# Kernel tuning notes

Measured on AMD Instinct MI355X. Metric: run time of the kernel, lower is better.

## Reference

```python
import jax, jax.numpy as jnp
import numpy as np

N = 100000      # number of entities
E = 400000      # number of edges (before self-loops)
D = 200         # feature_dim
D0 = 100        # init_fea_dim
NREL = 475      # 2*num_rels + 1 (self-loop relation = NREL-1)
NBR = 100       # num_base_r
B = 1024        # query batch
L = 2           # number of cells / layers
EPS = 1e-5


def _bn(x, g, b):
    # BatchNorm1d, training-mode batch statistics (biased var), per-feature affine
    m = jnp.mean(x, axis=0)
    v = jnp.var(x, axis=0)
    return (x - m) * jax.lax.rsqrt(v + EPS) * g + b


def setup_inputs() -> dict:
    key = jax.random.key(0)
    ks = jax.random.split(key, 12)
    return {
        # graph (edge list form of the DGL graph g)
        "src_id": jax.random.randint(ks[0], (E,), 0, N),
        "dst_id": jax.random.randint(ks[1], (E,), 0, N),
        "e_type": jax.random.randint(ks[2], (E,), 0, NREL - 1),  # NREL-1 reserved for self-loop
        # link-prediction queries
        "subj": jax.random.randint(ks[3], (B,), 0, N),
        "rel": jax.random.randint(ks[4], (B,), 0, NREL),
        # learned parameters
        "emb_h": jax.random.normal(ks[5], (N, D0), dtype=jnp.float32) * 0.02,
        "emb_e": jax.random.normal(ks[6], (NBR, D), dtype=jnp.float32) * 0.1,
        "lin_w": jax.random.normal(ks[7], (D0, D), dtype=jnp.float32) * (1.0 / np.sqrt(D0)),
        "lin_b": jnp.zeros((D,), dtype=jnp.float32),
        "rel_wt": jax.random.normal(ks[8], (NREL, NBR), dtype=jnp.float32) * 0.1,
        "w_rel": jax.random.normal(ks[9], (D, D), dtype=jnp.float32) * (1.0 / np.sqrt(D)),
        # per-cell params, stacked over L layers
        "agg_bn_g": jnp.ones((L, D), dtype=jnp.float32),
        "agg_bn_b": jnp.zeros((L, D), dtype=jnp.float32),
        "cell_bn_g": jnp.ones((L, D), dtype=jnp.float32),
        "cell_bn_b": jnp.zeros((L, D), dtype=jnp.float32),
        "concat_w": jax.random.normal(ks[10], (L, D, D), dtype=jnp.float32) * (1.0 / np.sqrt(D)),
        "concat_b": jnp.zeros((L, D), dtype=jnp.float32),
    }


def reference(src_id, dst_id, e_type, subj, rel,
              emb_h, emb_e, lin_w, lin_b, rel_wt, w_rel,
              agg_bn_g, agg_bn_b, cell_bn_g, cell_bn_b, concat_w, concat_b):
    nodes = jnp.arange(N, dtype=src_id.dtype)
    # append self-loops for every node, with the dedicated self-loop relation id
    src_f = jnp.concatenate([src_id, nodes])                      # [E+N]
    dst_f = jnp.concatenate([dst_id, nodes])                      # [E+N]
    et_f = jnp.concatenate([e_type, jnp.full((N,), NREL - 1, dtype=e_type.dtype)])

    all_ent = emb_h @ lin_w + lin_b                               # [N, D]
    rel_embed = rel_wt @ emb_e                                    # [NREL, D]

    for i in range(L):
        src_emb = all_ent[src_f]                                  # [E+N, D] per-edge gather
        hr = rel_embed[et_f]                                      # [E+N, D] per-edge gather
        zero_out = src_emb * hr                                   # pre_mult op (no BN/ReLU)
        agg = jax.ops.segment_sum(zero_out, dst_f, num_segments=N)  # edge -> node aggregation
        agg = jax.nn.relu(_bn(agg, agg_bn_g[i], agg_bn_b[i]))     # OpModule BN + ReLU
        h = agg @ concat_w[i] + concat_b[i]                       # Cell concat Linear (1 concat node)
        all_ent = jax.nn.relu(_bn(h, cell_bn_g[i], cell_bn_b[i]))  # Cell BN + ReLU
        rel_embed = rel_embed @ w_rel                             # per-layer relation transform

    # DistMult score function: [B, N]
    score = (all_ent[subj] * rel_embed[rel]) @ all_ent.T
    return score
```

## Files before the change

### kernel.cpp

```cpp
#include <hip/hip_runtime.h>


#define N_ENT  100000
#define N_EDGE 400000
#define D_     200
#define D0_    100
#define NREL_  475
#define B_     1024
#define GSTAT2 2048
#define KP_D   224
#define KP_D0  128

typedef unsigned short ushort_t;
typedef __attribute__((ext_vector_type(8))) short bf16x8;
typedef __attribute__((ext_vector_type(4))) float f32x4;

__device__ __forceinline__ ushort_t f2bf(float x) {
  unsigned u = __float_as_uint(x);
  return (ushort_t)((u + 0x7FFFu + ((u >> 16) & 1u)) >> 16);
}
__device__ __forceinline__ float bf2f(ushort_t h) {
  return __uint_as_float(((unsigned)h) << 16);
}

__device__ __forceinline__ void gld16(const void* g, void* l) {
  __builtin_amdgcn_global_load_lds(
      (const __attribute__((address_space(1))) unsigned*)g,
      (__attribute__((address_space(3))) unsigned*)l, 16, 0, 0);
}


__global__ void k_hist(const int* __restrict__ dst_id, int* __restrict__ cnt) {
  int e = blockIdx.x * 256 + threadIdx.x;
  if (e < N_EDGE) atomicAdd(&cnt[dst_id[e]], 1);
}

__global__ __launch_bounds__(256) void k_scan_block(const int* __restrict__ cnt,
                                                    int* __restrict__ rp,
                                                    int* __restrict__ bsum) {
  __shared__ int sm[256];
  int tid = threadIdx.x;
  int base = blockIdx.x * 1024 + tid * 4;
  int v0 = (base + 0 < N_ENT) ? cnt[base + 0] : 0;
  int v1 = (base + 1 < N_ENT) ? cnt[base + 1] : 0;
  int v2 = (base + 2 < N_ENT) ? cnt[base + 2] : 0;
  int v3 = (base + 3 < N_ENT) ? cnt[base + 3] : 0;
  int tsum = v0 + v1 + v2 + v3;
  sm[tid] = tsum;
  __syncthreads();
  for (int off = 1; off < 256; off <<= 1) {
    int t = (tid >= off) ? sm[tid - off] : 0;
    __syncthreads();
    sm[tid] += t;
    __syncthreads();
  }
  int run = sm[tid] - tsum;
  if (base + 0 < N_ENT) { rp[base + 0] = run; } run += v0;
  if (base + 1 < N_ENT) { rp[base + 1] = run; } run += v1;
  if (base + 2 < N_ENT) { rp[base + 2] = run; } run += v2;
  if (base + 3 < N_ENT) { rp[base + 3] = run; }
  if (tid == 255) bsum[blockIdx.x] = sm[255];
}

__global__ void k_scan_tops(int* __restrict__ bsum, int nb) {
  __shared__ int sm[256];
  int tid = threadIdx.x;
  int v = (tid < nb) ? bsum[tid] : 0;
  sm[tid] = v;
  __syncthreads();
  for (int off = 1; off < 256; off <<= 1) {
    int t = (tid >= off) ? sm[tid - off] : 0;
    __syncthreads();
    sm[tid] += t;
    __syncthreads();
  }
  if (tid < nb) bsum[tid] = sm[tid] - v;
}

__global__ void k_scan_add(int* __restrict__ rp, const int* __restrict__ bsum,
                           int* __restrict__ cursor) {
  int i = blockIdx.x * 256 + threadIdx.x;
  if (i < N_ENT) {
    int r = rp[i] + bsum[i >> 10];
    rp[i] = r;
    cursor[i] = r;
  }
}

__global__ void k_fill(const int* __restrict__ src_id, const int* __restrict__ dst_id,
                       const int* __restrict__ e_type, int* __restrict__ cursor,
                       int* __restrict__ cs, int* __restrict__ ct) {
  int e = blockIdx.x * 256 + threadIdx.x;
  if (e < N_EDGE) {
    int pos = atomicAdd(&cursor[dst_id[e]], 1);
    cs[pos] = src_id[e];
    ct[pos] = e_type[e];
  }
}


template <bool BN>
__global__ __launch_bounds__(256) void k_aggregate(const float* __restrict__ ent,
                                                   const float* __restrict__ relE,
                                                   const int* __restrict__ rp,
                                                   const int* __restrict__ cnt,
                                                   const int* __restrict__ cs,
                                                   const int* __restrict__ ct,
                                                   float* __restrict__ out,
                                                   const float* __restrict__ scale,
                                                   const float* __restrict__ shift) {
  int n = blockIdx.x;
  int f = threadIdx.x;
  if (f >= D_) return;
  float sc = 0.f, sh = 0.f;
  if (BN) { sc = scale[f]; sh = shift[f]; }
  float selfE = ent[(long)n * D_ + f];
  if (BN) selfE = fmaxf(fmaf(selfE, sc, sh), 0.f);
  float a0 = selfE * relE[(long)(NREL_ - 1) * D_ + f];
  float a1 = 0.f, a2 = 0.f, a3 = 0.f;
  int s0 = rp[n], e0 = s0 + cnt[n];
  int idx = s0;
  for (; idx + 4 <= e0; idx += 4) {
    int sA = cs[idx + 0], tA = ct[idx + 0];
    int sB = cs[idx + 1], tB = ct[idx + 1];
    int sC = cs[idx + 2], tC = ct[idx + 2];
    int sD = cs[idx + 3], tD = ct[idx + 3];
    float eA = ent[(long)sA * D_ + f], rA = relE[(long)tA * D_ + f];
    float eB = ent[(long)sB * D_ + f], rB = relE[(long)tB * D_ + f];
    float eC = ent[(long)sC * D_ + f], rC = relE[(long)tC * D_ + f];
    float eD = ent[(long)sD * D_ + f], rD = relE[(long)tD * D_ + f];
    if (BN) {
      eA = fmaxf(fmaf(eA, sc, sh), 0.f);
      eB = fmaxf(fmaf(eB, sc, sh), 0.f);
      eC = fmaxf(fmaf(eC, sc, sh), 0.f);
      eD = fmaxf(fmaf(eD, sc, sh), 0.f);
    }
    a0 = fmaf(eA, rA, a0);
    a1 = fmaf(eB, rB, a1);
    a2 = fmaf(eC, rC, a2);
    a3 = fmaf(eD, rD, a3);
  }
  for (; idx < e0; ++idx) {
    int sA = cs[idx], tA = ct[idx];
    float eA = ent[(long)sA * D_ + f];
    if (BN) eA = fmaxf(fmaf(eA, sc, sh), 0.f);
    a0 = fmaf(eA, relE[(long)tA * D_ + f], a0);
  }
  out[(long)n * D_ + f] = (a0 + a1) + (a2 + a3);
}

__global__ __launch_bounds__(64) void k_colstats(const float* __restrict__ X,
                                                 double* __restrict__ part) {
  int t = threadIdx.x;
  if (t >= 50) return;
  double s0 = 0, s1 = 0, s2 = 0, s3 = 0, q0 = 0, q1 = 0, q2 = 0, q3 = 0;
  for (int r = blockIdx.x; r < N_ENT; r += GSTAT2) {
    float4 v = *(const float4*)(X + (long)r * D_ + t * 4);
    s0 += v.x; q0 += (double)v.x * v.x;
    s1 += v.y; q1 += (double)v.y * v.y;
    s2 += v.z; q2 += (double)v.z * v.z;
    s3 += v.w; q3 += (double)v.w * v.w;
  }
  long o = (long)blockIdx.x * 400 + t * 4;
  part[o + 0] = s0; part[o + 1] = s1; part[o + 2] = s2; part[o + 3] = s3;
  part[o + 200] = q0; part[o + 201] = q1; part[o + 202] = q2; part[o + 203] = q3;
}

__global__ __launch_bounds__(256) void k_bn_fin(const double* __restrict__ part,
                                                const float* __restrict__ g,
                                                const float* __restrict__ b,
                                                float* __restrict__ scale,
                                                float* __restrict__ shift) {
  int f = blockIdx.x;
  int tid = threadIdx.x;
  double S = 0.0, S2 = 0.0;
  for (int i = tid; i < GSTAT2; i += 256) {
    S += part[(long)i * 400 + f];
    S2 += part[(long)i * 400 + 200 + f];
  }
  __shared__ double smS[256], smS2[256];
  smS[tid] = S; smS2[tid] = S2;
  __syncthreads();
  for (int off = 128; off > 0; off >>= 1) {
    if (tid < off) { smS[tid] += smS[tid + off]; smS2[tid] += smS2[tid + off]; }
    __syncthreads();
  }
  if (tid == 0) {
    double mean = smS[0] / N_ENT;
    double var = smS2[0] / N_ENT - mean * mean;
    double inv = 1.0 / sqrt(var + 1e-5);
    float sc = g[f] * (float)inv;
    scale[f] = sc;
    shift[f] = b[f] - (float)mean * sc;
  }
}

__global__ void k_norm_split(float* __restrict__ X, const float* __restrict__ scale,
                             const float* __restrict__ shift,
                             ushort_t* __restrict__ H, ushort_t* __restrict__ L) {
  const long total = (long)N_ENT * (KP_D / 4);
  for (long i4 = (long)blockIdx.x * 256 + threadIdx.x; i4 < total;
       i4 += (long)gridDim.x * 256) {
    int r = (int)(i4 / (KP_D / 4));
    int c4 = (int)(i4 % (KP_D / 4)) * 4;
    float vv[4] = {0.f, 0.f, 0.f, 0.f};
    if (c4 < D_) {
      float4 v = *(float4*)(X + (long)r * D_ + c4);
      vv[0] = fmaxf(fmaf(v.x, scale[c4 + 0], shift[c4 + 0]), 0.f);
      vv[1] = fmaxf(fmaf(v.y, scale[c4 + 1], shift[c4 + 1]), 0.f);
      vv[2] = fmaxf(fmaf(v.z, scale[c4 + 2], shift[c4 + 2]), 0.f);
      vv[3] = fmaxf(fmaf(v.w, scale[c4 + 3], shift[c4 + 3]), 0.f);
      *(float4*)(X + (long)r * D_ + c4) = make_float4(vv[0], vv[1], vv[2], vv[3]);
    }
    ushort_t h[4], l[4];
#pragma unroll
    for (int t = 0; t < 4; t++) {
      h[t] = f2bf(vv[t]);
      l[t] = f2bf(vv[t] - bf2f(h[t]));
    }
    long o = (long)r * KP_D + c4;
    *(uint2*)(H + o) = make_uint2((unsigned)h[0] | ((unsigned)h[1] << 16),
                                  (unsigned)h[2] | ((unsigned)h[3] << 16));
    *(uint2*)(L + o) = make_uint2((unsigned)l[0] | ((unsigned)l[1] << 16),
                                  (unsigned)l[2] | ((unsigned)l[3] << 16));
  }
}

__global__ void k_tsplit(const float* __restrict__ W, int K, int Nc, int Kp,
                         ushort_t* __restrict__ H, ushort_t* __restrict__ L) {
  int i = blockIdx.x * 256 + threadIdx.x;
  if (i >= Nc * Kp) return;
  int n = i / Kp, kp = i - n * Kp;
  float v = (kp < K) ? W[(long)kp * Nc + n] : 0.f;
  ushort_t h = f2bf(v);
  H[i] = h;
  L[i] = f2bf(v - bf2f(h));
}

__global__ void k_qsplit(const float* __restrict__ ent, const float* __restrict__ relE,
                         const int* __restrict__ subj, const int* __restrict__ rel,
                         ushort_t* __restrict__ H, ushort_t* __restrict__ L) {
  int i = blockIdx.x * 256 + threadIdx.x;
  if (i >= B_ * KP_D) return;
  int b = i / KP_D, kp = i - b * KP_D;
  float v = 0.f;
  if (kp < D_)
    v = ent[(long)subj[b] * D_ + kp] * relE[(long)rel[b] * D_ + kp];
  ushort_t h = f2bf(v);
  H[i] = h;
  L[i] = f2bf(v - bf2f(h));
}

template <bool SWZ>
__global__ __launch_bounds__(256, 2) void k_score(
    const ushort_t* __restrict__ Ah, const ushort_t* __restrict__ Al,
    const ushort_t* __restrict__ Bh, const ushort_t* __restrict__ Bl,
    float* __restrict__ C, int M, int Nc, long ldc) {
  constexpr int KP = KP_D;
  constexpr int NT = KP / 32;
  __shared__ __align__(16) ushort_t lds[2 * 12288];
  const int tid = threadIdx.x;
  const int wave = tid >> 6, lane = tid & 63;
  int bxi, byi;
  if (SWZ) {
    int orig = blockIdx.x;
    int cpx = gridDim.x >> 3;
    int swz = (orig & 7) * cpx + (orig >> 3);
    bxi = swz & 15;
    byi = swz >> 4;
  } else {
    bxi = blockIdx.x;
    byi = blockIdx.y;
  }
  const int bm = bxi * 64, bn = byi * 128;
  const int wr = (wave >> 1) * 32, wc = (wave & 1) * 64;
  const int l15 = lane & 15, l4 = lane >> 4;

  f32x4 acc[2][4] = {};

  auto stage = [&](int kt, int ph) {
#pragma unroll
    for (int j = 0; j < 6; ++j) {
      int c = wave * 6 + j;
      int r;
      const ushort_t* bp;
      int rowg;
      if (c < 4)       { r = c * 16 + (lane >> 2);        bp = Ah; rowg = bm + r; }
      else if (c < 8)  { r = (c - 4) * 16 + (lane >> 2);  bp = Al; rowg = bm + r; }
      else if (c < 16) { r = (c - 8) * 16 + (lane >> 2);  bp = Bh; rowg = bn + r; if (rowg > Nc - 1) rowg = Nc - 1; }
      else             { r = (c - 16) * 16 + (lane >> 2); bp = Bl; rowg = bn + r; if (rowg > Nc - 1) rowg = Nc - 1; }
      int sg = (lane & 3) ^ ((r >> 1) & 3);
      gld16(bp + (long)rowg * KP + kt * 32 + sg * 8, lds + ph * 12288 + c * 512);
    }
  };

  stage(0, 0);
  __syncthreads();
  int p = 0;
#pragma unroll
  for (int t = 0; t < NT; ++t) {
    if (t + 1 < NT) stage(t + 1, p ^ 1);
    const ushort_t* base = lds + p * 12288;
    bf16x8 a_h[2], a_l[2], b_h[4], b_l[4];
#pragma unroll
    for (int i = 0; i < 2; i++) {
      int rA = wr + i * 16 + l15;
      int s = (l4 ^ ((rA >> 1) & 3)) * 8;
      a_h[i] = *(const bf16x8*)(base + rA * 32 + s);
      a_l[i] = *(const bf16x8*)(base + 2048 + rA * 32 + s);
    }
#pragma unroll
    for (int j = 0; j < 4; j++) {
      int rB = wc + j * 16 + l15;
      int s = (l4 ^ ((rB >> 1) & 3)) * 8;
      b_h[j] = *(const bf16x8*)(base + 4096 + rB * 32 + s);
      b_l[j] = *(const bf16x8*)(base + 8192 + rB * 32 + s);
    }
#pragma unroll
    for (int i = 0; i < 2; i++)
#pragma unroll
      for (int j = 0; j < 4; j++) {
        acc[i][j] = __builtin_amdgcn_mfma_f32_16x16x32_bf16(a_h[i], b_h[j], acc[i][j], 0, 0, 0);
        acc[i][j] = __builtin_amdgcn_mfma_f32_16x16x32_bf16(a_l[i], b_h[j], acc[i][j], 0, 0, 0);
        acc[i][j] = __builtin_amdgcn_mfma_f32_16x16x32_bf16(a_h[i], b_l[j], acc[i][j], 0, 0, 0);
      }
    __syncthreads();
    p ^= 1;
  }

#pragma unroll
  for (int i = 0; i < 2; i++) {
    int mrow = bm + wr + i * 16 + l4 * 4;
#pragma unroll
    for (int j = 0; j < 4; j++) {
      int n = bn + wc + j * 16 + l15;
      if (n >= Nc) continue;
#pragma unroll
      for (int v = 0; v < 4; v++) {
        int m = mrow + v;
        if (m < M) C[(long)m * ldc + n] = acc[i][j][v];
      }
    }
  }
}

template <bool BN_A, bool HAS_BIAS>
__global__ __launch_bounds__(256, 2) void k_mfma_af32(
    const float* __restrict__ A, int lda, int K,
    const ushort_t* __restrict__ Bh, const ushort_t* __restrict__ Bl,
    float* __restrict__ C, int M, int Nc, int Kp, long ldc,
    const float* __restrict__ scale, const float* __restrict__ shift,
    const float* __restrict__ bias) {
  __shared__ __align__(16) ushort_t lds[2 * 16384];
  __shared__ float sc_lds[KP_D], sh_lds[KP_D];
  const int tid = threadIdx.x;
  const int wave = tid >> 6, lane = tid & 63;
  const int bm = blockIdx.x * 128, bn = blockIdx.y * 128;
  const int wr = (wave >> 1) * 64, wc = (wave & 1) * 64;
  const int l15 = lane & 15, l4 = lane >> 4;
  const int NT = Kp >> 5;

  if (BN_A) {
    for (int i = tid; i < Kp; i += 256) {
      sc_lds[i] = (i < K) ? scale[i] : 0.f;
      sh_lds[i] = (i < K) ? shift[i] : 0.f;
    }
    __syncthreads();
  }

  const int ar = tid >> 1;
  const int acb = (tid & 1) * 16;
  int arow = bm + ar; if (arow > M - 1) arow = M - 1;
  const int aswz = (ar >> 1) & 3;
  const int s0 = (((acb >> 3) + 0) ^ aswz) * 8;
  const int s1 = (((acb >> 3) + 1) ^ aswz) * 8;

  auto loadA = [&](int kt, float4* va) {
    int kc = kt * 32 + acb;
    const float* ap = A + (long)arow * lda + kc;
    if (kc + 16 <= K) {
#pragma unroll
      for (int q = 0; q < 4; q++) va[q] = *(const float4*)(ap + q * 4);
    } else {
#pragma unroll
      for (int q = 0; q < 4; q++) {
        float t0 = (kc + q * 4 + 0 < K) ? ap[q * 4 + 0] : 0.f;
        float t1 = (kc + q * 4 + 1 < K) ? ap[q * 4 + 1] : 0.f;
        float t2 = (kc + q * 4 + 2 < K) ? ap[q * 4 + 2] : 0.f;
        float t3 = (kc + q * 4 + 3 < K) ? ap[q * 4 + 3] : 0.f;
        va[q] = make_float4(t0, t1, t2, t3);
      }
    }
  };

  auto writeA = [&](int kt, int ph, float4* va) {
    float v[16];
#pragma unroll
    for (int q = 0; q < 4; q++) {
      v[q * 4 + 0] = va[q].x; v[q * 4 + 1] = va[q].y;
      v[q * 4 + 2] = va[q].z; v[q * 4 + 3] = va[q].w;
    }
    if (BN_A) {
      int kc = kt * 32 + acb;
#pragma unroll
      for (int e = 0; e < 16; e++) {
        int col = kc + e;
        if (col < K) v[e] = fmaxf(fmaf(v[e], sc_lds[col], sh_lds[col]), 0.f);
      }
    }
    unsigned hh[8], ll[8];
#pragma unroll
    for (int e = 0; e < 8; e++) {
      ushort_t h0 = f2bf(v[2 * e]), h1 = f2bf(v[2 * e + 1]);
      ushort_t l0 = f2bf(v[2 * e] - bf2f(h0)), l1 = f2bf(v[2 * e + 1] - bf2f(h1));
      hh[e] = (unsigned)h0 | ((unsigned)h1 << 16);
      ll[e] = (unsigned)l0 | ((unsigned)l1 << 16);
    }
    ushort_t* baseA = lds + ph * 16384 + ar * 32;
    *(uint4*)(baseA + s0) = make_uint4(hh[0], hh[1], hh[2], hh[3]);
    *(uint4*)(baseA + s1) = make_uint4(hh[4], hh[5], hh[6], hh[7]);
    ushort_t* baseL = baseA + 4096;
    *(uint4*)(baseL + s0) = make_uint4(ll[0], ll[1], ll[2], ll[3]);
    *(uint4*)(baseL + s1) = make_uint4(ll[4], ll[5], ll[6], ll[7]);
  };

  auto stageB = [&](int kt, int ph) {
#pragma unroll
    for (int j = 0; j < 4; ++j) {
      int c = 16 + wave * 4 + j;
      int buf = c >> 3;
      int r = (c & 7) * 16 + (lane >> 2);
      int sg = (lane & 3) ^ ((r >> 1) & 3);
      const ushort_t* bp = (buf == 2) ? Bh : Bl;
      int rowg = bn + r; if (rowg > Nc - 1) rowg = Nc - 1;
      gld16(bp + (long)rowg * Kp + kt * 32 + sg * 8, lds + ph * 16384 + c * 512);
    }
  };

  f32x4 acc[4][4] = {};
  {
    float4 va[4];
    loadA(0, va);
    writeA(0, 0, va);
    stageB(0, 0);
  }
  __syncthreads();
  int p = 0;
  for (int t = 0; t < NT; ++t) {
    float4 va[4];
    const bool pre = (t + 1 < NT);
    if (pre) {
      loadA(t + 1, va);
      stageB(t + 1, p ^ 1);
    }
    const ushort_t* base = lds + p * 16384;
    bf16x8 a_h[4], a_l[4], b_h[4], b_l[4];
#pragma unroll
    for (int i = 0; i < 4; i++) {
      int rA = wr + i * 16 + l15;
      int sA = (l4 ^ ((rA >> 1) & 3)) * 8;
      a_h[i] = *(const bf16x8*)(base + rA * 32 + sA);
      a_l[i] = *(const bf16x8*)(base + 4096 + rA * 32 + sA);
      int rB = wc + i * 16 + l15;
      int sB = (l4 ^ ((rB >> 1) & 3)) * 8;
      b_h[i] = *(const bf16x8*)(base + 8192 + rB * 32 + sB);
      b_l[i] = *(const bf16x8*)(base + 12288 + rB * 32 + sB);
    }
#pragma unroll
    for (int i = 0; i < 4; i++)
#pragma unroll
      for (int j = 0; j < 4; j++) {
        acc[i][j] = __builtin_amdgcn_mfma_f32_16x16x32_bf16(a_h[i], b_h[j], acc[i][j], 0, 0, 0);
        acc[i][j] = __builtin_amdgcn_mfma_f32_16x16x32_bf16(a_l[i], b_h[j], acc[i][j], 0, 0, 0);
        acc[i][j] = __builtin_amdgcn_mfma_f32_16x16x32_bf16(a_h[i], b_l[j], acc[i][j], 0, 0, 0);
      }
    if (pre) writeA(t + 1, p ^ 1, va);
    __syncthreads();
    p ^= 1;
  }

#pragma unroll
  for (int i = 0; i < 4; i++) {
    int mrow = bm + wr + i * 16 + l4 * 4;
#pragma unroll
    for (int j = 0; j < 4; j++) {
      int n = bn + wc + j * 16 + l15;
      if (n >= Nc) continue;
      float bb = HAS_BIAS ? bias[n] : 0.f;
#pragma unroll
      for (int v = 0; v < 4; v++) {
        int m = mrow + v;
        if (m < M) C[(long)m * ldc + n] = acc[i][j][v] + bb;
      }
    }
  }
}

template <int TM, int TN>
__global__ __launch_bounds__(256) void k_gemm_abt(
    const float* __restrict__ A, const float* __restrict__ Bm, float* __restrict__ C,
    int M, int Nc, int K, long ldc) {
  constexpr int BM = TM * 16, BN = TN * 16, KC = 20;
  __shared__ float As[BM * KC];
  __shared__ float Bs[BN * KC];
  const int tid = threadIdx.x;
  const int tx = tid & 15, ty = tid >> 4;
  const int bm = blockIdx.x * BM, bn = blockIdx.y * BN;
  float acc[TM][TN];
#pragma unroll
  for (int i = 0; i < TM; i++)
#pragma unroll
    for (int j = 0; j < TN; j++) acc[i][j] = 0.f;
  for (int kc = 0; kc < K; kc += KC) {
    for (int i4 = tid; i4 < BM * 5; i4 += 256) {
      int r = i4 / 5, kq = (i4 - r * 5) * 4;
      int row = bm + r; if (row > M - 1) row = M - 1;
      *(float4*)(As + r * KC + kq) = *(const float4*)(A + (long)row * K + kc + kq);
    }
    for (int i4 = tid; i4 < BN * 5; i4 += 256) {
      int r = i4 / 5, kq = (i4 - r * 5) * 4;
      int row = bn + r; if (row > Nc - 1) row = Nc - 1;
      *(float4*)(Bs + r * KC + kq) = *(const float4*)(Bm + (long)row * K + kc + kq);
    }
    __syncthreads();
#pragma unroll
    for (int k4 = 0; k4 < KC; k4 += 4) {
      float4 af[TM], bf[TN];
#pragma unroll
      for (int i = 0; i < TM; i++) af[i] = *(const float4*)(As + (i * 16 + ty) * KC + k4);
#pragma unroll
      for (int j = 0; j < TN; j++) bf[j] = *(const float4*)(Bs + (j * 16 + tx) * KC + k4);
#pragma unroll
      for (int i = 0; i < TM; i++)
#pragma unroll
        for (int j = 0; j < TN; j++) {
          acc[i][j] = fmaf(af[i].x, bf[j].x, acc[i][j]);
          acc[i][j] = fmaf(af[i].y, bf[j].y, acc[i][j]);
          acc[i][j] = fmaf(af[i].z, bf[j].z, acc[i][j]);
          acc[i][j] = fmaf(af[i].w, bf[j].w, acc[i][j]);
        }
    }
    __syncthreads();
  }
#pragma unroll
  for (int i = 0; i < TM; i++) {
    int m = bm + i * 16 + ty;
    if (m >= M) continue;
#pragma unroll
    for (int j = 0; j < TN; j++) {
      int n = bn + j * 16 + tx;
      if (n < Nc) C[(long)m * ldc + n] = acc[i][j];
    }
  }
}

__global__ void k_transpose(const float* __restrict__ s, float* __restrict__ d, int R, int C) {
  int i = blockIdx.x * 256 + threadIdx.x;
  if (i < R * C) { int r = i / C, c = i - r * C; d[c * R + r] = s[i]; }
}


extern "C" void kernel_launch(void* const* d_in, const int* in_sizes, int n_in,
                              void* d_out, int out_size, void* d_ws, size_t ws_size,
                              hipStream_t stream) {
  const int* src_id = (const int*)d_in[0];
  const int* dst_id = (const int*)d_in[1];
  const int* e_type = (const int*)d_in[2];
  const int* subj = (const int*)d_in[3];
  const int* rel = (const int*)d_in[4];
  const float* emb_h = (const float*)d_in[5];
  const float* emb_e = (const float*)d_in[6];
  const float* lin_w = (const float*)d_in[7];
  const float* lin_b = (const float*)d_in[8];
  const float* rel_wt = (const float*)d_in[9];
  const float* w_rel = (const float*)d_in[10];
  const float* agg_bn_g = (const float*)d_in[11];
  const float* agg_bn_b = (const float*)d_in[12];
  const float* cell_bn_g = (const float*)d_in[13];
  const float* cell_bn_b = (const float*)d_in[14];
  const float* concat_w = (const float*)d_in[15];
  const float* concat_b = (const float*)d_in[16];
  float* out = (float*)d_out;

  char* w = (char*)d_ws;
  ushort_t* ent_h = (ushort_t*)(w + 0);
  ushort_t* ent_l = (ushort_t*)(w + 44800000);
  ushort_t* q_h   = (ushort_t*)(w + 89600000);
  ushort_t* q_l   = (ushort_t*)(w + 90112000);

  char* ob = (char*)d_out;
  float* ent    = (float*)(ob + 0);
  float* tmp    = (float*)(ob + 80000000);
  double* part  = (double*)(ob + 160000000);
  int* counts   = (int*)(ob + 166600000);
  int* row_ptr  = (int*)(ob + 167000000);
  int* cursor   = (int*)(ob + 167400000);
  int* csr_src  = (int*)(ob + 167800000);
  int* csr_et   = (int*)(ob + 169400000);
  float* relA   = (float*)(ob + 171800000);
  float* relB   = (float*)(ob + 172180000);
  float* embeT  = (float*)(ob + 172560000);
  float* wrT    = (float*)(ob + 172640000);
  ushort_t* linw_h = (ushort_t*)(ob + 172800000);
  ushort_t* linw_l = (ushort_t*)(ob + 172851200);
  ushort_t* cw0_h  = (ushort_t*)(ob + 172902400);
  ushort_t* cw0_l  = (ushort_t*)(ob + 172992000);
  ushort_t* cw1_h  = (ushort_t*)(ob + 173081600);
  ushort_t* cw1_l  = (ushort_t*)(ob + 173171200);
  float* scaleb = (float*)(ob + 173260800);
  float* shiftb = (float*)(ob + 173261824);
  int* bsum     = (int*)(ob + 173262848);

  hipMemsetAsync(counts, 0, N_ENT * sizeof(int), stream);
  k_hist<<<(N_EDGE + 255) / 256, 256, 0, stream>>>(dst_id, counts);
  const int NB = (N_ENT + 1023) / 1024;
  k_scan_block<<<NB, 256, 0, stream>>>(counts, row_ptr, bsum);
  k_scan_tops<<<1, 256, 0, stream>>>(bsum, NB);
  k_scan_add<<<(N_ENT + 255) / 256, 256, 0, stream>>>(row_ptr, bsum, cursor);
  k_fill<<<(N_EDGE + 255) / 256, 256, 0, stream>>>(src_id, dst_id, e_type, cursor,
                                                   csr_src, csr_et);

  k_tsplit<<<(D_ * KP_D0 + 255) / 256, 256, 0, stream>>>(lin_w, D0_, D_, KP_D0,
                                                         linw_h, linw_l);
  k_tsplit<<<(D_ * KP_D + 255) / 256, 256, 0, stream>>>(concat_w, D_, D_, KP_D,
                                                        cw0_h, cw0_l);
  k_tsplit<<<(D_ * KP_D + 255) / 256, 256, 0, stream>>>(concat_w + D_ * D_, D_, D_,
                                                        KP_D, cw1_h, cw1_l);
  k_transpose<<<(D0_ * D_ + 255) / 256, 256, 0, stream>>>(emb_e, embeT, D0_, D_);
  k_transpose<<<(D_ * D_ + 255) / 256, 256, 0, stream>>>(w_rel, wrT, D_, D_);

  const int GM = (N_ENT + 127) / 128;

  k_mfma_af32<false, true><<<dim3(GM, 2), 256, 0, stream>>>(
      emb_h, D0_, D0_, linw_h, linw_l, ent, N_ENT, D_, KP_D0, (long)D_,
      nullptr, nullptr, lin_b);
  k_gemm_abt<8, 4><<<dim3(4, 4), 256, 0, stream>>>(rel_wt, embeT, relA, NREL_, D_,
                                                   D0_, (long)D_);

  k_aggregate<false><<<N_ENT, 256, 0, stream>>>(ent, relA, row_ptr, counts,
                                                csr_src, csr_et, tmp, nullptr, nullptr);
  k_colstats<<<GSTAT2, 64, 0, stream>>>(tmp, part);
  k_bn_fin<<<D_, 256, 0, stream>>>(part, agg_bn_g, agg_bn_b, scaleb, shiftb);
  k_mfma_af32<true, true><<<dim3(GM, 2), 256, 0, stream>>>(
      tmp, D_, D_, cw0_h, cw0_l, ent, N_ENT, D_, KP_D, (long)D_,
      scaleb, shiftb, concat_b);
  k_colstats<<<GSTAT2, 64, 0, stream>>>(ent, part);
  k_bn_fin<<<D_, 256, 0, stream>>>(part, cell_bn_g, cell_bn_b, scaleb, shiftb);
  k_gemm_abt<8, 4><<<dim3(4, 4), 256, 0, stream>>>(relA, wrT, relB, NREL_, D_, D_,
                                                   (long)D_);

  k_aggregate<true><<<N_ENT, 256, 0, stream>>>(ent, relB, row_ptr, counts,
                                               csr_src, csr_et, tmp, scaleb, shiftb);
  k_colstats<<<GSTAT2, 64, 0, stream>>>(tmp, part);
  k_bn_fin<<<D_, 256, 0, stream>>>(part, agg_bn_g + D_, agg_bn_b + D_, scaleb, shiftb);
  k_mfma_af32<true, true><<<dim3(GM, 2), 256, 0, stream>>>(
      tmp, D_, D_, cw1_h, cw1_l, ent, N_ENT, D_, KP_D, (long)D_,
      scaleb, shiftb, concat_b + D_);
  k_colstats<<<GSTAT2, 64, 0, stream>>>(ent, part);
  k_bn_fin<<<D_, 256, 0, stream>>>(part, cell_bn_g + D_, cell_bn_b + D_, scaleb, shiftb);
  k_norm_split<<<2048, 256, 0, stream>>>(ent, scaleb, shiftb, ent_h, ent_l);
  k_gemm_abt<8, 4><<<dim3(4, 4), 256, 0, stream>>>(relB, wrT, relA, NREL_, D_, D_,
                                                   (long)D_);

  k_qsplit<<<(B_ * KP_D + 255) / 256, 256, 0, stream>>>(ent, relA, subj, rel,
                                                        q_h, q_l);

  k_score<true><<<dim3((B_ / 64) * GM), 256, 0, stream>>>(
      q_h, q_l, ent_h, ent_l, out, B_, N_ENT, (long)N_ENT);
}
```

Before: 1.131 ms.

## Restructure score GEMM to keep entity tile resident and stream all queries

The DistMult score kernel is rewritten so each block loads a 64-entity slab of the split-bf16 entity matrix (full K) into LDS once. It then loops over all 1024 queries in 64-row chunks, reading query fragments straight from global memory, which are shared across blocks through cache. This removes the repeated entity loads and the per-K-step double-buffer synchronisation of the old 64x128 tiled kernel. In exchange, per-block work is serialized over 16 chunks, there is no prefetch overlap for the A loads, and register pressure rises from holding 14 A fragments per row tile.

Result: faster. 1.091 ms (-3.5%).

```diff
diff --git a/kernel.cpp b/kernel.cpp
--- a/kernel.cpp
+++ b/kernel.cpp
@@ -251,94 +251,77 @@
   L[i] = f2bf(v - bf2f(h));
 }
 
-template <bool SWZ>
-__global__ __launch_bounds__(256, 2) void k_score(
+__global__ __launch_bounds__(256, 2) void k_score2(
     const ushort_t* __restrict__ Ah, const ushort_t* __restrict__ Al,
     const ushort_t* __restrict__ Bh, const ushort_t* __restrict__ Bl,
-    float* __restrict__ C, int M, int Nc, long ldc) {
+    float* __restrict__ C) {
   constexpr int KP = KP_D;
-  constexpr int NT = KP / 32;
-  __shared__ __align__(16) ushort_t lds[2 * 12288];
+  __shared__ __align__(16) ushort_t lds[2 * 14336];
   const int tid = threadIdx.x;
   const int wave = tid >> 6, lane = tid & 63;
-  int bxi, byi;
-  if (SWZ) {
-    int orig = blockIdx.x;
-    int cpx = gridDim.x >> 3;
-    int swz = (orig & 7) * cpx + (orig >> 3);
-    bxi = swz & 15;
-    byi = swz >> 4;
-  } else {
-    bxi = blockIdx.x;
-    byi = blockIdx.y;
-  }
-  const int bm = bxi * 64, bn = byi * 128;
-  const int wr = (wave >> 1) * 32, wc = (wave & 1) * 64;
   const int l15 = lane & 15, l4 = lane >> 4;
-
-  f32x4 acc[2][4] = {};
-
-  auto stage = [&](int kt, int ph) {
-#pragma unroll
-    for (int j = 0; j < 6; ++j) {
-      int c = wave * 6 + j;
-      int r;
-      const ushort_t* bp;
-      int rowg;
-      if (c < 4)       { r = c * 16 + (lane >> 2);        bp = Ah; rowg = bm + r; }
-      else if (c < 8)  { r = (c - 4) * 16 + (lane >> 2);  bp = Al; rowg = bm + r; }
-      else if (c < 16) { r = (c - 8) * 16 + (lane >> 2);  bp = Bh; rowg = bn + r; if (rowg > Nc - 1) rowg = Nc - 1; }
-      else             { r = (c - 16) * 16 + (lane >> 2); bp = Bl; rowg = bn + r; if (rowg > Nc - 1) rowg = Nc - 1; }
-      int sg = (lane & 3) ^ ((r >> 1) & 3);
-      gld16(bp + (long)rowg * KP + kt * 32 + sg * 8, lds + ph * 12288 + c * 512);
-    }
-  };
-
-  stage(0, 0);
+  const int bn = blockIdx.x * 64;
+  const int wm = wave >> 1, wn = wave & 1;
+
+#pragma unroll
+  for (int jj = 0; jj < 14; ++jj) {
+    int c = wave * 14 + jj;
+    int u = c * 64 + lane;
+    int isl = (u >= 1792) ? 1 : 0;
+    int u2 = u - isl * 1792;
+    int kst = u2 >> 8;
+    int rem = u2 & 255;
+    int r = rem >> 2;
+    int slot = rem & 3;
+    int srcslot = slot ^ ((r >> 1) & 3);
+    int rowg = bn + r; if (rowg > N_ENT - 1) rowg = N_ENT - 1;
+    const ushort_t* src = (isl ? Bl : Bh) + (long)rowg * KP + kst * 32 + srcslot * 8;
+    gld16(src, lds + c * 512);
+  }
   __syncthreads();
-  int p = 0;
-#pragma unroll
-  for (int t = 0; t < NT; ++t) {
-    if (t + 1 < NT) stage(t + 1, p ^ 1);
-    const ushort_t* base = lds + p * 12288;
-    bf16x8 a_h[2], a_l[2], b_h[4], b_l[4];
-#pragma unroll
-    for (int i = 0; i < 2; i++) {
-      int rA = wr + i * 16 + l15;
-      int s = (l4 ^ ((rA >> 1) & 3)) * 8;
-      a_h[i] = *(const bf16x8*)(base + rA * 32 + s);
-      a_l[i] = *(const bf16x8*)(base + 2048 + rA * 32 + s);
-    }
-#pragma unroll
-    for (int j = 0; j < 4; j++) {
-      int rB = wc + j * 16 + l15;
-      int s = (l4 ^ ((rB >> 1) & 3)) * 8;
-      b_h[j] = *(const bf16x8*)(base + 4096 + rB * 32 + s);
-      b_l[j] = *(const bf16x8*)(base + 8192 + rB * 32 + s);
-    }
-#pragma unroll
-    for (int i = 0; i < 2; i++)
-#pragma unroll
-      for (int j = 0; j < 4; j++) {
-        acc[i][j] = __builtin_amdgcn_mfma_f32_16x16x32_bf16(a_h[i], b_h[j], acc[i][j], 0, 0, 0);
-        acc[i][j] = __builtin_amdgcn_mfma_f32_16x16x32_bf16(a_l[i], b_h[j], acc[i][j], 0, 0, 0);
-        acc[i][j] = __builtin_amdgcn_mfma_f32_16x16x32_bf16(a_h[i], b_l[j], acc[i][j], 0, 0, 0);
+
+  for (int mi = 0; mi < 16; ++mi) {
+    bf16x8 ah[2][7], al[2][7];
+#pragma unroll
+    for (int i = 0; i < 2; ++i) {
+      long rowa = (long)(mi * 64 + wm * 32 + i * 16 + l15) * KP + l4 * 8;
+#pragma unroll
+      for (int k = 0; k < 7; ++k) {
+        ah[i][k] = *(const bf16x8*)(Ah + rowa + k * 32);
+        al[i][k] = *(const bf16x8*)(Al + rowa + k * 32);
       }
-    __syncthreads();
-    p ^= 1;
-  }
-
-#pragma unroll
-  for (int i = 0; i < 2; i++) {
-    int mrow = bm + wr + i * 16 + l4 * 4;
-#pragma unroll
-    for (int j = 0; j < 4; j++) {
-      int n = bn + wc + j * 16 + l15;
-      if (n >= Nc) continue;
-#pragma unroll
-      for (int v = 0; v < 4; v++) {
-        int m = mrow + v;
-        if (m < M) C[(long)m * ldc + n] = acc[i][j][v];
+    }
+    f32x4 acc[2][2] = {};
+#pragma unroll
+    for (int k = 0; k < 7; ++k) {
+      bf16x8 bh[2], bl[2];
+#pragma unroll
+      for (int j = 0; j < 2; ++j) {
+        int rB = wn * 32 + j * 16 + l15;
+        int slot = l4 ^ ((rB >> 1) & 3);
+        int ad = k * 2048 + rB * 32 + slot * 8;
+        bh[j] = *(const bf16x8*)(lds + ad);
+        bl[j] = *(const bf16x8*)(lds + 14336 + ad);
+      }
+#pragma unroll
+      for (int i = 0; i < 2; ++i)
+#pragma unroll
+        for (int j = 0; j < 2; ++j) {
+          acc[i][j] = __builtin_amdgcn_mfma_f32_16x16x32_bf16(ah[i][k], bh[j], acc[i][j], 0, 0, 0);
+          acc[i][j] = __builtin_amdgcn_mfma_f32_16x16x32_bf16(al[i][k], bh[j], acc[i][j], 0, 0, 0);
+          acc[i][j] = __builtin_amdgcn_mfma_f32_16x16x32_bf16(ah[i][k], bl[j], acc[i][j], 0, 0, 0);
+        }
+    }
+#pragma unroll
+    for (int i = 0; i < 2; ++i) {
+      int m0 = mi * 64 + wm * 32 + i * 16 + l4 * 4;
+#pragma unroll
+      for (int j = 0; j < 2; ++j) {
+        int n = bn + wn * 32 + j * 16 + l15;
+        if (n >= N_ENT) continue;
+#pragma unroll
+        for (int v = 0; v < 4; ++v)
+          C[(long)(m0 + v) * N_ENT + n] = acc[i][j][v];
       }
     }
   }
@@ -665,6 +648,5 @@
   k_qsplit<<<(B_ * KP_D + 255) / 256, 256, 0, stream>>>(ent, relA, subj, rel,
                                                         q_h, q_l);
 
-  k_score<true><<<dim3((B_ / 64) * GM), 256, 0, stream>>>(
-      q_h, q_l, ent_h, ent_l, out, B_, N_ENT, (long)N_ENT);
-}
+  k_score2<<<dim3((N_ENT + 63) / 64), 256, 0, stream>>>(q_h, q_l, ent_h, ent_l, out);
+}
```
